# Kernel tuning notes

Measured on AMD Instinct MI355X. Metric: run time of the kernel, lower is better.

The kernel has to match this reference:

```python
import jax, jax.numpy as jnp
import numpy as np

B = 131072


def _unfold3(x):
    # torch F.unfold(kernel=3, stride=1, pad=0), feature order (c, kh, kw)
    Bn, C, H, W = x.shape
    Ho, Wo = H - 2, W - 2
    cols = [x[:, :, i:i + Ho, j:j + Wo] for i in range(3) for j in range(3)]
    p = jnp.stack(cols, axis=2)  # (B, C, 9, Ho, Wo)
    return p.reshape(Bn, C * 9, Ho, Wo)


def setup_inputs() -> dict:
    key = jax.random.key(0)
    ks = jax.random.split(key, 7)
    return {
        "x": jax.random.uniform(ks[0], (B, 1, 9, 9), dtype=jnp.float32),
        "w1": jax.random.normal(ks[1], (16, 9), dtype=jnp.float32) * 0.3,
        "b1": jax.random.normal(ks[2], (16,), dtype=jnp.float32) * 0.1,
        "w2": jax.random.normal(ks[3], (32, 144), dtype=jnp.float32) * 0.1,
        "b2": jax.random.normal(ks[4], (32,), dtype=jnp.float32) * 0.1,
        "fc_w": jax.random.normal(ks[5], (4, 32), dtype=jnp.float32) * 0.2,
        "fc_b": jax.random.normal(ks[6], (4,), dtype=jnp.float32) * 0.1,
    }


def reference(x, w1, b1, w2, b2, fc_w, fc_b):
    # LogicConv2d #1: unfold -> per-out-channel optical unit (batched as one einsum)
    p1 = _unfold3(x)  # (B, 9, 7, 7)
    h1 = jax.nn.sigmoid(jnp.einsum('bdhw,od->bohw', p1, w1) + b1[None, :, None, None])
    h1 = jax.nn.relu(h1)
    # MaxPool2d(2,2), floor mode: 7x7 -> 3x3
    h1 = jax.lax.reduce_window(h1, -jnp.inf, jax.lax.max,
                               (1, 1, 2, 2), (1, 1, 2, 2), 'VALID')
    # LogicConv2d #2: 3x3x16 -> 1x1x32
    p2 = _unfold3(h1)  # (B, 144, 1, 1)
    h2 = jax.nn.sigmoid(jnp.einsum('bdhw,od->bohw', p2, w2) + b2[None, :, None, None])
    # flatten + fc
    flat = h2.reshape(h2.shape[0], -1)  # (B, 32)
    return flat @ fc_w.T + fc_b
```

## Files before the change

kernel.cpp:

```cpp
#include <hip/hip_runtime.h>
#include <hip/hip_bf16.h>
#include <math.h>


typedef float v2f __attribute__((ext_vector_type(2)));
typedef float f4  __attribute__((ext_vector_type(4)));
typedef f4 uf4 __attribute__((aligned(4)));
typedef __bf16 bf16x2 __attribute__((ext_vector_type(2)));
typedef __bf16 bf16x8 __attribute__((ext_vector_type(8)));
typedef float f32x16 __attribute__((ext_vector_type(16)));
typedef unsigned int u32;
typedef u32 u32x2 __attribute__((ext_vector_type(2)));
typedef u32 u32x4 __attribute__((ext_vector_type(4)));

#define BLOCK 256
#define LOG2E 1.4426950408889634f

#define OFF_SMALL 2304
#define S_W1P  0
#define S_B1P  144
#define S_FCWP 160
#define S_B2S  288
#define SMALL_FLOATS 320
#define PREP_ITEMS (4608 + SMALL_FLOATS)

__device__ __forceinline__ float sig2(float s) {
    return __builtin_amdgcn_rcpf(1.0f + __builtin_amdgcn_exp2f(-s));
}

__global__ void prep_kernel(const float* __restrict__ w1,
                            const float* __restrict__ b1,
                            const float* __restrict__ w2,
                            const float* __restrict__ b2,
                            const float* __restrict__ fcw,
                            float* __restrict__ ws) {
    int i = blockIdx.x * blockDim.x + threadIdx.x;
    if (i < 4608) {
        int j = i & 7, lane = (i >> 3) & 63, kb = (i >> 9) % 3, pi = i / 1536;
        int k = kb * 16 + (lane >> 5) * 8 + j;
        int o = k / 3, pj = k - 3 * o;
        float v = w2[(lane & 31) * 144 + o * 9 + pi * 3 + pj] * LOG2E;
        ((__bf16*)ws)[i] = (__bf16)v;
    } else if (i < PREP_ITEMS) {
        int r = i - 4608;
        float v;
        if (r < S_B1P) {
            int h = r & 1, k = (r >> 1) % 9, op = (r >> 1) / 9;
            v = w1[(2 * op + h) * 9 + k] * LOG2E;
        } else if (r < S_FCWP) {
            int q = r - S_B1P;
            v = b1[2 * (q >> 1) + (q & 1)] * LOG2E;
        } else if (r < S_B2S) {
            int q = r - S_FCWP;
            int h = q & 1, j = (q >> 1) % 16, rr = (q >> 1) / 16;
            v = fcw[rr * 32 + 2 * j + h];
        } else {
            v = b2[r - S_B2S] * LOG2E;
        }
        ws[OFF_SMALL + r] = v;
    }
}

__global__ __launch_bounds__(BLOCK, 2) void olcnn_kernel(
    const float* __restrict__ xg,
    const float* __restrict__ wsf,
    const float* __restrict__ fcb,
    float* __restrict__ out)
{
    __shared__ u32 lds_scr[4 * 2176];
    __shared__ __align__(16) float lws[SMALL_FLOATS];

    const int tid  = threadIdx.x;
    const int lane = tid & 63;
    const int wid  = tid >> 6;
    u32* scr = lds_scr + wid * 2176;

    if (tid < SMALL_FLOATS / 4)
        ((f4*)lws)[tid] = ((const f4*)(wsf + OFF_SMALL))[tid];
    __syncthreads();

    const v2f* w1p  = (const v2f*)(lws + S_W1P);
    const v2f* b1p  = (const v2f*)(lws + S_B1P);
    const v2f* fcwp = (const v2f*)(lws + S_FCWP);

    const int t = blockIdx.x * BLOCK + tid;
    const float* xs = xg + (long long)t * 81;

    const u32x4* bfrag_g = (const u32x4*)wsf;

    f32x16 acc0{};
    f32x16 acc1{};

    const int m0  = lane & 31;
    const int kha = (lane >> 5) * 4;

    #pragma unroll 1
    for (int pi = 0; pi < 3; ++pi) {
        float xb[4][8];
        #pragma unroll
        for (int r = 0; r < 4; ++r) {
            const float* rp = xs + (2 * pi + r) * 9;
            f4 a = *(const uf4*)rp;
            f4 b = *(const uf4*)(rp + 4);
            xb[r][0] = a.x; xb[r][1] = a.y; xb[r][2] = a.z; xb[r][3] = a.w;
            xb[r][4] = b.x; xb[r][5] = b.y; xb[r][6] = b.z; xb[r][7] = b.w;
        }
        #pragma unroll
        for (int r = 0; r < 4; ++r)
            #pragma unroll
            for (int c = 0; c < 8; ++c)
                asm volatile("" : "+v"(xb[r][c]));

        float p48[48];
        #pragma unroll
        for (int op = 0; op < 8; ++op) {
            v2f wv[9];
            #pragma unroll
            for (int k = 0; k < 9; ++k) wv[k] = w1p[op * 9 + k];
            const v2f bb = b1p[op];
            #pragma unroll
            for (int pj = 0; pj < 3; ++pj) {
                v2f vmax;
                #pragma unroll
                for (int dh = 0; dh < 2; ++dh)
                    #pragma unroll
                    for (int dw = 0; dw < 2; ++dw) {
                        v2f s = bb;
                        #pragma unroll
                        for (int i = 0; i < 3; ++i)
                            #pragma unroll
                            for (int jj = 0; jj < 3; ++jj) {
                                float xv = xb[dh + i][2 * pj + dw + jj];
                                s = __builtin_elementwise_fma(
                                        (v2f){xv, xv}, wv[i * 3 + jj], s);
                            }
                        if (dh == 0 && dw == 0) vmax = s;
                        else vmax = __builtin_elementwise_max(vmax, s);
                    }
                p48[(2 * op) * 3 + pj]     = sig2(vmax.x);
                p48[(2 * op + 1) * 3 + pj] = sig2(vmax.y);
            }
        }

        #pragma unroll
        for (int q = 0; q < 24; ++q) {
            bf16x2 hp;
            hp.x = (__bf16)p48[2 * q];
            hp.y = (__bf16)p48[2 * q + 1];
            scr[lane * 26 + q] = __builtin_bit_cast(u32, hp);
        }

        #pragma unroll
        for (int kb = 0; kb < 3; ++kb) {
            u32x4 bw = bfrag_g[(pi * 3 + kb) * 64 + lane];
            bf16x8 bf = __builtin_bit_cast(bf16x8, bw);

            const int off = kb * 8 + kha;
            u32x2 a0l = *(const u32x2*)(scr + m0 * 26 + off);
            u32x2 a0h = *(const u32x2*)(scr + m0 * 26 + off + 2);
            u32x2 a1l = *(const u32x2*)(scr + (m0 + 32) * 26 + off);
            u32x2 a1h = *(const u32x2*)(scr + (m0 + 32) * 26 + off + 2);
            u32x4 aw0; aw0.x = a0l.x; aw0.y = a0l.y; aw0.z = a0h.x; aw0.w = a0h.y;
            u32x4 aw1; aw1.x = a1l.x; aw1.y = a1l.y; aw1.z = a1h.x; aw1.w = a1h.y;

            acc0 = __builtin_amdgcn_mfma_f32_32x32x16_bf16(
                       __builtin_bit_cast(bf16x8, aw0), bf, acc0, 0, 0, 0);
            acc1 = __builtin_amdgcn_mfma_f32_32x32x16_bf16(
                       __builtin_bit_cast(bf16x8, aw1), bf, acc1, 0, 0, 0);
        }
    }

    const float b2v = lws[S_B2S + (lane & 31)];
    #pragma unroll
    for (int r = 0; r < 16; ++r) {
        const int srow = (r & 3) + 8 * (r >> 2) + 4 * (lane >> 5);
        scr[srow * 34 + (lane & 31)] =
            __builtin_bit_cast(u32, sig2(acc0[r] + b2v));
        scr[(srow + 32) * 34 + (lane & 31)] =
            __builtin_bit_cast(u32, sig2(acc1[r] + b2v));
    }

    v2f h2[16];
    #pragma unroll
    for (int j = 0; j < 16; ++j)
        h2[j] = *(const v2f*)((const float*)scr + lane * 34 + 2 * j);

    v2f a0 = h2[0] * fcwp[0],  a1 = h2[0] * fcwp[16],
        a2 = h2[0] * fcwp[32], a3 = h2[0] * fcwp[48];
    #pragma unroll
    for (int j = 1; j < 16; ++j) {
        a0 = __builtin_elementwise_fma(h2[j], fcwp[0 * 16 + j], a0);
        a1 = __builtin_elementwise_fma(h2[j], fcwp[1 * 16 + j], a1);
        a2 = __builtin_elementwise_fma(h2[j], fcwp[2 * 16 + j], a2);
        a3 = __builtin_elementwise_fma(h2[j], fcwp[3 * 16 + j], a3);
    }
    ((float4*)out)[t] = make_float4(fcb[0] + a0.x + a0.y,
                                    fcb[1] + a1.x + a1.y,
                                    fcb[2] + a2.x + a2.y,
                                    fcb[3] + a3.x + a3.y);
}

extern "C" void kernel_launch(void* const* d_in, const int* in_sizes, int n_in,
                              void* d_out, int out_size, void* d_ws, size_t ws_size,
                              hipStream_t stream) {
    const float* x   = (const float*)d_in[0];
    const float* w1  = (const float*)d_in[1];
    const float* b1  = (const float*)d_in[2];
    const float* w2  = (const float*)d_in[3];
    const float* b2  = (const float*)d_in[4];
    const float* fcw = (const float*)d_in[5];
    const float* fcb = (const float*)d_in[6];
    float* out = (float*)d_out;
    float* ws  = (float*)d_ws;

    prep_kernel<<<dim3((PREP_ITEMS + 255) / 256), dim3(256), 0, stream>>>(
        w1, b1, w2, b2, fcw, ws);

    const int nB = in_sizes[0] / 81;
    olcnn_kernel<<<dim3(nB / BLOCK), dim3(BLOCK), 0, stream>>>(x, ws, fcb, out);
}
```

Baseline: 107.9 us.

## Prefetch next input rows, preload B fragments, and replace LDS A-staging with lane shuffles

Result: slower. 113.6 us (+5.4%).

```diff
diff --git a/kernel.cpp b/kernel.cpp
--- a/kernel.cpp
+++ b/kernel.cpp
@@ -10,7 +10,6 @@
 typedef __bf16 bf16x8 __attribute__((ext_vector_type(8)));
 typedef float f32x16 __attribute__((ext_vector_type(16)));
 typedef unsigned int u32;
-typedef u32 u32x2 __attribute__((ext_vector_type(2)));
 typedef u32 u32x4 __attribute__((ext_vector_type(4)));
 
 #define BLOCK 256
@@ -26,6 +25,11 @@
 
 __device__ __forceinline__ float sig2(float s) {
     return __builtin_amdgcn_rcpf(1.0f + __builtin_amdgcn_exp2f(-s));
+}
+
+__device__ __forceinline__ u32 pack_bf(float a, float b) {
+    bf16x2 p; p.x = (__bf16)a; p.y = (__bf16)b;
+    return __builtin_bit_cast(u32, p);
 }
 
 __global__ void prep_kernel(const float* __restrict__ w1,
@@ -61,6 +65,20 @@
     }
 }
 
+#define LOADB(dst, pi_)                                              \
+    do {                                                             \
+        _Pragma("unroll")                                            \
+        for (int r_ = 0; r_ < 4; ++r_) {                             \
+            const float* rp_ = xs + (2 * (pi_) + r_) * 9;            \
+            f4 a_ = *(const uf4*)rp_;                                \
+            f4 b_ = *(const uf4*)(rp_ + 4);                          \
+            dst[r_][0] = a_.x; dst[r_][1] = a_.y;                    \
+            dst[r_][2] = a_.z; dst[r_][3] = a_.w;                    \
+            dst[r_][4] = b_.x; dst[r_][5] = b_.y;                    \
+            dst[r_][6] = b_.z; dst[r_][7] = b_.w;                    \
+        }                                                            \
+    } while (0)
+
 __global__ __launch_bounds__(BLOCK, 2) void olcnn_kernel(
     const float* __restrict__ xg,
     const float* __restrict__ wsf,
@@ -87,37 +105,39 @@
     const float* xs = xg + (long long)t * 81;
 
     const u32x4* bfrag_g = (const u32x4*)wsf;
+    u32x4 bfr[9];
+    #pragma unroll
+    for (int q = 0; q < 9; ++q) bfr[q] = bfrag_g[q * 64 + lane];
 
     f32x16 acc0{};
     f32x16 acc1{};
 
-    const int m0  = lane & 31;
-    const int kha = (lane >> 5) * 4;
+    const bool h0 = (lane < 32);
+
+    float xb[4][8], xbn[4][8];
+    LOADB(xbn, 0);
 
     #pragma unroll 1
     for (int pi = 0; pi < 3; ++pi) {
-        float xb[4][8];
-        #pragma unroll
-        for (int r = 0; r < 4; ++r) {
-            const float* rp = xs + (2 * pi + r) * 9;
-            f4 a = *(const uf4*)rp;
-            f4 b = *(const uf4*)(rp + 4);
-            xb[r][0] = a.x; xb[r][1] = a.y; xb[r][2] = a.z; xb[r][3] = a.w;
-            xb[r][4] = b.x; xb[r][5] = b.y; xb[r][6] = b.z; xb[r][7] = b.w;
-        }
         #pragma unroll
         for (int r = 0; r < 4; ++r)
             #pragma unroll
-            for (int c = 0; c < 8; ++c)
-                asm volatile("" : "+v"(xb[r][c]));
-
-        float p48[48];
+            for (int c = 0; c < 8; ++c) {
+                float v = xbn[r][c];
+                asm volatile("" : "+v"(v));
+                xb[r][c] = v;
+            }
+        if (pi < 2) LOADB(xbn, pi + 1);
+        __builtin_amdgcn_sched_barrier(0);
+
+        u32 pk[24];
         #pragma unroll
         for (int op = 0; op < 8; ++op) {
             v2f wv[9];
             #pragma unroll
             for (int k = 0; k < 9; ++k) wv[k] = w1p[op * 9 + k];
             const v2f bb = b1p[op];
+            v2f vm[3];
             #pragma unroll
             for (int pj = 0; pj < 3; ++pj) {
                 v2f vmax;
@@ -137,32 +157,30 @@
                         if (dh == 0 && dw == 0) vmax = s;
                         else vmax = __builtin_elementwise_max(vmax, s);
                     }
-                p48[(2 * op) * 3 + pj]     = sig2(vmax.x);
-                p48[(2 * op + 1) * 3 + pj] = sig2(vmax.y);
+                vm[pj] = vmax;
             }
-        }
-
-        #pragma unroll
-        for (int q = 0; q < 24; ++q) {
-            bf16x2 hp;
-            hp.x = (__bf16)p48[2 * q];
-            hp.y = (__bf16)p48[2 * q + 1];
-            scr[lane * 26 + q] = __builtin_bit_cast(u32, hp);
+            float s00 = sig2(vm[0].x), s01 = sig2(vm[1].x), s02 = sig2(vm[2].x);
+            float s10 = sig2(vm[0].y), s11 = sig2(vm[1].y), s12 = sig2(vm[2].y);
+            pk[3 * op + 0] = pack_bf(s00, s01);
+            pk[3 * op + 1] = pack_bf(s02, s10);
+            pk[3 * op + 2] = pack_bf(s11, s12);
         }
 
         #pragma unroll
         for (int kb = 0; kb < 3; ++kb) {
-            u32x4 bw = bfrag_g[(pi * 3 + kb) * 64 + lane];
-            bf16x8 bf = __builtin_bit_cast(bf16x8, bw);
-
-            const int off = kb * 8 + kha;
-            u32x2 a0l = *(const u32x2*)(scr + m0 * 26 + off);
-            u32x2 a0h = *(const u32x2*)(scr + m0 * 26 + off + 2);
-            u32x2 a1l = *(const u32x2*)(scr + (m0 + 32) * 26 + off);
-            u32x2 a1h = *(const u32x2*)(scr + (m0 + 32) * 26 + off + 2);
-            u32x4 aw0; aw0.x = a0l.x; aw0.y = a0l.y; aw0.z = a0h.x; aw0.w = a0h.y;
-            u32x4 aw1; aw1.x = a1l.x; aw1.y = a1l.y; aw1.z = a1h.x; aw1.w = a1h.y;
-
+            u32 a0d[4], a1d[4];
+            #pragma unroll
+            for (int i = 0; i < 4; ++i) {
+                u32 lo = pk[kb * 8 + i];
+                u32 hi = pk[kb * 8 + 4 + i];
+                u32 s  = h0 ? hi : lo;
+                u32 tt = (u32)__shfl_xor((int)s, 32);
+                a0d[i] = h0 ? lo : tt;
+                a1d[i] = h0 ? tt : hi;
+            }
+            u32x4 aw0; aw0.x = a0d[0]; aw0.y = a0d[1]; aw0.z = a0d[2]; aw0.w = a0d[3];
+            u32x4 aw1; aw1.x = a1d[0]; aw1.y = a1d[1]; aw1.z = a1d[2]; aw1.w = a1d[3];
+            bf16x8 bf = __builtin_bit_cast(bf16x8, bfr[pi * 3 + kb]);
             acc0 = __builtin_amdgcn_mfma_f32_32x32x16_bf16(
                        __builtin_bit_cast(bf16x8, aw0), bf, acc0, 0, 0, 0);
             acc1 = __builtin_amdgcn_mfma_f32_32x32x16_bf16(
```

## Split each sample across two lanes and feed MFMA via cross-lane shuffles

Applied to the files above, without the earlier changes.

Measured after the change: 110.2 us. 2.2% more time.

```diff
diff --git a/kernel.cpp b/kernel.cpp
--- a/kernel.cpp
+++ b/kernel.cpp
@@ -10,7 +10,6 @@
 typedef __bf16 bf16x8 __attribute__((ext_vector_type(8)));
 typedef float f32x16 __attribute__((ext_vector_type(16)));
 typedef unsigned int u32;
-typedef u32 u32x2 __attribute__((ext_vector_type(2)));
 typedef u32 u32x4 __attribute__((ext_vector_type(4)));
 
 #define BLOCK 256
@@ -26,6 +25,11 @@
 
 __device__ __forceinline__ float sig2(float s) {
     return __builtin_amdgcn_rcpf(1.0f + __builtin_amdgcn_exp2f(-s));
+}
+
+__device__ __forceinline__ u32 pack_bf(float a, float b) {
+    bf16x2 p; p.x = (__bf16)a; p.y = (__bf16)b;
+    return __builtin_bit_cast(u32, p);
 }
 
 __global__ void prep_kernel(const float* __restrict__ w1,
@@ -61,19 +65,24 @@
     }
 }
 
-__global__ __launch_bounds__(BLOCK, 2) void olcnn_kernel(
+__global__ __launch_bounds__(BLOCK)
+__attribute__((amdgpu_waves_per_eu(4, 4)))
+void olcnn_kernel(
     const float* __restrict__ xg,
     const float* __restrict__ wsf,
     const float* __restrict__ fcb,
     float* __restrict__ out)
 {
-    __shared__ u32 lds_scr[4 * 2176];
+    __shared__ u32 lds_scr[4 * 1088];
     __shared__ __align__(16) float lws[SMALL_FLOATS];
 
     const int tid  = threadIdx.x;
     const int lane = tid & 63;
     const int wid  = tid >> 6;
-    u32* scr = lds_scr + wid * 2176;
+    const int h    = lane >> 5;
+    const bool h0  = (h == 0);
+    const int s    = lane & 31;
+    u32* scr = lds_scr + wid * 1088;
 
     if (tid < SMALL_FLOATS / 4)
         ((f4*)lws)[tid] = ((const f4*)(wsf + OFF_SMALL))[tid];
@@ -83,16 +92,12 @@
     const v2f* b1p  = (const v2f*)(lws + S_B1P);
     const v2f* fcwp = (const v2f*)(lws + S_FCWP);
 
-    const int t = blockIdx.x * BLOCK + tid;
-    const float* xs = xg + (long long)t * 81;
+    const int samp = blockIdx.x * 128 + wid * 32 + s;
+    const float* xs = xg + (long long)samp * 81;
 
     const u32x4* bfrag_g = (const u32x4*)wsf;
 
-    f32x16 acc0{};
-    f32x16 acc1{};
-
-    const int m0  = lane & 31;
-    const int kha = (lane >> 5) * 4;
+    f32x16 acc{};
 
     #pragma unroll 1
     for (int pi = 0; pi < 3; ++pi) {
@@ -111,13 +116,20 @@
             for (int c = 0; c < 8; ++c)
                 asm volatile("" : "+v"(xb[r][c]));
 
-        float p48[48];
-        #pragma unroll
-        for (int op = 0; op < 8; ++op) {
+        u32x4 bfr[3];
+        #pragma unroll
+        for (int kb = 0; kb < 3; ++kb)
+            bfr[kb] = bfrag_g[(pi * 3 + kb) * 64 + lane];
+
+        u32 pk[12];
+        #pragma unroll
+        for (int opl = 0; opl < 4; ++opl) {
+            const int gop = 4 * h + opl;
             v2f wv[9];
             #pragma unroll
-            for (int k = 0; k < 9; ++k) wv[k] = w1p[op * 9 + k];
-            const v2f bb = b1p[op];
+            for (int k = 0; k < 9; ++k) wv[k] = w1p[gop * 9 + k];
+            const v2f bb = b1p[gop];
+            v2f vm[3];
             #pragma unroll
             for (int pj = 0; pj < 3; ++pj) {
                 v2f vmax;
@@ -125,79 +137,71 @@
                 for (int dh = 0; dh < 2; ++dh)
                     #pragma unroll
                     for (int dw = 0; dw < 2; ++dw) {
-                        v2f s = bb;
+                        v2f sacc = bb;
                         #pragma unroll
                         for (int i = 0; i < 3; ++i)
                             #pragma unroll
                             for (int jj = 0; jj < 3; ++jj) {
                                 float xv = xb[dh + i][2 * pj + dw + jj];
-                                s = __builtin_elementwise_fma(
-                                        (v2f){xv, xv}, wv[i * 3 + jj], s);
+                                sacc = __builtin_elementwise_fma(
+                                           (v2f){xv, xv}, wv[i * 3 + jj], sacc);
                             }
-                        if (dh == 0 && dw == 0) vmax = s;
-                        else vmax = __builtin_elementwise_max(vmax, s);
+                        if (dh == 0 && dw == 0) vmax = sacc;
+                        else vmax = __builtin_elementwise_max(vmax, sacc);
                     }
-                p48[(2 * op) * 3 + pj]     = sig2(vmax.x);
-                p48[(2 * op + 1) * 3 + pj] = sig2(vmax.y);
+                vm[pj] = vmax;
             }
-        }
-
-        #pragma unroll
-        for (int q = 0; q < 24; ++q) {
-            bf16x2 hp;
-            hp.x = (__bf16)p48[2 * q];
-            hp.y = (__bf16)p48[2 * q + 1];
-            scr[lane * 26 + q] = __builtin_bit_cast(u32, hp);
-        }
+            float s00 = sig2(vm[0].x), s01 = sig2(vm[1].x), s02 = sig2(vm[2].x);
+            float s10 = sig2(vm[0].y), s11 = sig2(vm[1].y), s12 = sig2(vm[2].y);
+            pk[3 * opl + 0] = pack_bf(s00, s01);
+            pk[3 * opl + 1] = pack_bf(s02, s10);
+            pk[3 * opl + 2] = pack_bf(s11, s12);
+        }
+
+        u32 recv[4];
+        #pragma unroll
+        for (int i = 0; i < 4; ++i)
+            recv[i] = (u32)__shfl_xor((int)pk[4 + i], 32);
 
         #pragma unroll
         for (int kb = 0; kb < 3; ++kb) {
-            u32x4 bw = bfrag_g[(pi * 3 + kb) * 64 + lane];
-            bf16x8 bf = __builtin_bit_cast(bf16x8, bw);
-
-            const int off = kb * 8 + kha;
-            u32x2 a0l = *(const u32x2*)(scr + m0 * 26 + off);
-            u32x2 a0h = *(const u32x2*)(scr + m0 * 26 + off + 2);
-            u32x2 a1l = *(const u32x2*)(scr + (m0 + 32) * 26 + off);
-            u32x2 a1h = *(const u32x2*)(scr + (m0 + 32) * 26 + off + 2);
-            u32x4 aw0; aw0.x = a0l.x; aw0.y = a0l.y; aw0.z = a0h.x; aw0.w = a0h.y;
-            u32x4 aw1; aw1.x = a1l.x; aw1.y = a1l.y; aw1.z = a1h.x; aw1.w = a1h.y;
-
-            acc0 = __builtin_amdgcn_mfma_f32_32x32x16_bf16(
-                       __builtin_bit_cast(bf16x8, aw0), bf, acc0, 0, 0, 0);
-            acc1 = __builtin_amdgcn_mfma_f32_32x32x16_bf16(
-                       __builtin_bit_cast(bf16x8, aw1), bf, acc1, 0, 0, 0);
-        }
-    }
-
-    const float b2v = lws[S_B2S + (lane & 31)];
+            u32 ad[4];
+            #pragma unroll
+            for (int i = 0; i < 4; ++i) {
+                ad[i] = (kb == 0) ? (h0 ? pk[i]     : recv[i])
+                      : (kb == 1) ? (h0 ? pk[8 + i] : pk[i])
+                                  : (h0 ? recv[i]   : pk[8 + i]);
+            }
+            u32x4 aw; aw.x = ad[0]; aw.y = ad[1]; aw.z = ad[2]; aw.w = ad[3];
+            acc = __builtin_amdgcn_mfma_f32_32x32x16_bf16(
+                      __builtin_bit_cast(bf16x8, aw),
+                      __builtin_bit_cast(bf16x8, bfr[kb]), acc, 0, 0, 0);
+        }
+    }
+
+    const float b2v = lws[S_B2S + s];
     #pragma unroll
     for (int r = 0; r < 16; ++r) {
-        const int srow = (r & 3) + 8 * (r >> 2) + 4 * (lane >> 5);
-        scr[srow * 34 + (lane & 31)] =
-            __builtin_bit_cast(u32, sig2(acc0[r] + b2v));
-        scr[(srow + 32) * 34 + (lane & 31)] =
-            __builtin_bit_cast(u32, sig2(acc1[r] + b2v));
+        const int srow = (r & 3) + 8 * (r >> 2) + 4 * h;
+        scr[srow * 34 + s] = __builtin_bit_cast(u32, sig2(acc[r] + b2v));
     }
 
     v2f h2[16];
     #pragma unroll
     for (int j = 0; j < 16; ++j)
-        h2[j] = *(const v2f*)((const float*)scr + lane * 34 + 2 * j);
-
-    v2f a0 = h2[0] * fcwp[0],  a1 = h2[0] * fcwp[16],
-        a2 = h2[0] * fcwp[32], a3 = h2[0] * fcwp[48];
+        h2[j] = *(const v2f*)((const float*)scr + s * 34 + 2 * j);
+
+    const v2f* fA = fcwp + (2 * h) * 16;
+    const v2f* fB = fcwp + (2 * h + 1) * 16;
+    v2f aA = h2[0] * fA[0], aB = h2[0] * fB[0];
     #pragma unroll
     for (int j = 1; j < 16; ++j) {
-        a0 = __builtin_elementwise_fma(h2[j], fcwp[0 * 16 + j], a0);
-        a1 = __builtin_elementwise_fma(h2[j], fcwp[1 * 16 + j], a1);
-        a2 = __builtin_elementwise_fma(h2[j], fcwp[2 * 16 + j], a2);
-        a3 = __builtin_elementwise_fma(h2[j], fcwp[3 * 16 + j], a3);
-    }
-    ((float4*)out)[t] = make_float4(fcb[0] + a0.x + a0.y,
-                                    fcb[1] + a1.x + a1.y,
-                                    fcb[2] + a2.x + a2.y,
-                                    fcb[3] + a3.x + a3.y);
+        aA = __builtin_elementwise_fma(h2[j], fA[j], aA);
+        aB = __builtin_elementwise_fma(h2[j], fB[j], aB);
+    }
+    float2 res = make_float2(fcb[2 * h] + aA.x + aA.y,
+                             fcb[2 * h + 1] + aB.x + aB.y);
+    ((float2*)out)[samp * 2 + h] = res;
 }
 
 extern "C" void kernel_launch(void* const* d_in, const int* in_sizes, int n_in,
@@ -217,5 +221,5 @@
         w1, b1, w2, b2, fcw, ws);
 
     const int nB = in_sizes[0] / 81;
-    olcnn_kernel<<<dim3(nB / BLOCK), dim3(BLOCK), 0, stream>>>(x, ws, fcb, out);
-}
+    olcnn_kernel<<<dim3(nB / 128), dim3(BLOCK), 0, stream>>>(x, ws, fcb, out);
+}
```
